# Optimization experiments

Hardware: AMD Instinct MI355X
Metric: run time of the kernel (lower is better)

## Reference

```python
import jax, jax.numpy as jnp
import numpy as np

N_NODES = 100000
NUM_LAYER = 3
REG_WEIGHT = 1e-4


def setup_inputs() -> dict:
    key = jax.random.key(0)
    ks = jax.random.split(key, 6)
    E = 1280000
    B = 4096
    D = 64
    # xavier-uniform-like scale for embedding table
    emb_weight = jax.random.normal(ks[0], (N_NODES, D), dtype=jnp.float32) * 0.01
    src = jax.random.randint(ks[1], (E,), 0, N_NODES, dtype=jnp.int32)
    dst = jax.random.randint(ks[2], (E,), 0, N_NODES, dtype=jnp.int32)
    users = jax.random.randint(ks[3], (B,), 0, N_NODES, dtype=jnp.int32)
    pos = jax.random.randint(ks[4], (B,), 0, N_NODES, dtype=jnp.int32)
    neg = jax.random.randint(ks[5], (B,), 0, N_NODES, dtype=jnp.int32)
    return {"emb_weight": emb_weight, "src": src, "dst": dst,
            "users": users, "pos": pos, "neg": neg}


def _edge_norm(src, dst):
    # DGL norm(): d = sum of edge mask (ones) per dst node; adj_e = d[src]^-0.5 * d[dst]^-0.5
    ones = jnp.ones(src.shape[0], dtype=jnp.float32)
    deg = jax.ops.segment_sum(ones, dst, num_segments=N_NODES)
    dinv = jnp.where(deg > 0, deg ** -0.5, 0.0)  # inf -> 0 handling
    return dinv[src] * dinv[dst]  # [E]


def _propagate(emb_weight, src, dst, adj):
    # LightGCN propagation: h_{l+1}[v] = sum_{(u->v)} adj_e * h_l[u]
    h = emb_weight
    layers = [h]
    for _ in range(NUM_LAYER):
        m = h[src] * adj[:, None]                    # [E, D] gather + edge weight
        h = jax.ops.segment_sum(m, dst, num_segments=N_NODES)  # [N, D] scatter-sum
        layers.append(h)
    return jnp.mean(jnp.stack(layers, axis=1), axis=1)  # mean over L+1 layers


def reference(emb_weight, src, dst, users, pos, neg):
    adj = _edge_norm(src, dst)
    all_emb = _propagate(emb_weight, src, dst, adj)

    u_e, p_e, n_e = all_emb[users], all_emb[pos], all_emb[neg]
    u0, p0, n0 = emb_weight[users], emb_weight[pos], emb_weight[neg]

    B = users.shape[0]
    reg_loss = 0.5 * (jnp.sum(u0 ** 2) + jnp.sum(p0 ** 2) + jnp.sum(n0 ** 2)) / B
    reg_loss = reg_loss * REG_WEIGHT

    pos_scores = jnp.sum(u_e * p_e, axis=1)
    neg_scores = jnp.sum(u_e * n_e, axis=1)
    loss_emb = jnp.mean(jax.nn.softplus(neg_scores - pos_scores))

    loss = loss_emb + reg_loss
    return loss, loss_emb, reg_loss
```

## Files before the change

### kernel.cpp

```cpp
#include <hip/hip_runtime.h>
#include <hip/hip_fp8.h>
#include <math.h>

#define N_NODES 100000
#define DIM 64
#define NUM_LAYER 3
#define BATCH 4096
#define REG_WEIGHT 1e-4f
#define NBUCKET 391
#define STAGE_CAP 4096
#define CURPAD 16
#define H_SCALE 64.0f
#define H_INV_SCALE (1.0f / 64.0f)

__device__ unsigned char g_hf8[2][(size_t)N_NODES * DIM];
__device__ float g_sums[(size_t)3 * BATCH * DIM];
__device__ int   g_row_ptr[N_NODES + 1];
__device__ float g_dinv[N_NODES];
__device__ int   g_bcur[NBUCKET * CURPAD];
__device__ unsigned int g_stage[NBUCKET * STAGE_CAP];
__device__ int2  g_csr[1280000];
__device__ float g_part_sp[BATCH];
__device__ float g_part_rg[BATCH];

__device__ inline float fp8_to_f32(unsigned int v) {
    __hip_fp8_e4m3 t; t.__x = (__hip_fp8_storage_t)(v & 0xFF); return (float)t;
}
__device__ inline unsigned int f32_to_fp8(float f) {
    __hip_fp8_e4m3 t(f); return (unsigned int)t.__x;
}

__global__ void prelude(const float* __restrict__ emb,
                        const int* __restrict__ users, const int* __restrict__ pos,
                        const int* __restrict__ neg) {
    int i = blockIdx.x * blockDim.x + threadIdx.x;
    int stride = gridDim.x * blockDim.x;
    for (int k = i; k < NBUCKET; k += stride) g_bcur[k * CURPAD] = k * STAGE_CAP;
    const int NW = N_NODES * DIM / 4;
    unsigned int* hw = (unsigned int*)g_hf8[0];
    for (int k = i; k < NW; k += stride) {
        const float* e = emb + (size_t)k * 4;
        hw[k] = f32_to_fp8(e[0] * H_SCALE)         | (f32_to_fp8(e[1] * H_SCALE) << 8) |
                (f32_to_fp8(e[2] * H_SCALE) << 16) | (f32_to_fp8(e[3] * H_SCALE) << 24);
    }
    for (int k = i; k < 3 * BATCH * DIM; k += stride) {
        int wid = k >> 6, lane = k & 63;
        int which = wid / BATCH, s = wid - which * BATCH;
        const int* idx = (which == 0) ? users : ((which == 1) ? pos : neg);
        g_sums[k] = emb[(size_t)idx[s] * DIM + lane];
    }
}

#define EDGES_PER_THREAD 8
__global__ void __launch_bounds__(1024) stage_buckets(const int* __restrict__ src,
                                                      const int* __restrict__ dst, int E) {
    __shared__ int h[NBUCKET];
    __shared__ int cur[NBUCKET];
    int tid = threadIdx.x;
    int base = blockIdx.x * (1024 * EDGES_PER_THREAD);
    for (int i = tid; i < NBUCKET; i += 1024) h[i] = 0;
    __syncthreads();
    int myd[EDGES_PER_THREAD], mys[EDGES_PER_THREAD];
    #pragma unroll
    for (int k = 0; k < EDGES_PER_THREAD; ++k) {
        int e = base + k * 1024 + tid;
        if (e < E) {
            myd[k] = dst[e]; mys[k] = src[e];
            atomicAdd(&h[myd[k] >> 8], 1);
        } else myd[k] = -1;
    }
    __syncthreads();
    for (int i = tid; i < NBUCKET; i += 1024) {
        int c = h[i];
        cur[i] = c ? atomicAdd(&g_bcur[i * CURPAD], c) : 0;
    }
    __syncthreads();
    #pragma unroll
    for (int k = 0; k < EDGES_PER_THREAD; ++k) {
        if (myd[k] >= 0) {
            int p = atomicAdd(&cur[myd[k] >> 8], 1);
            g_stage[p] = (unsigned int)((mys[k] << 8) | (myd[k] & 255));
        }
    }
}

__global__ void __launch_bounds__(512) bucket_finalize() {
    __shared__ int cs[512];
    __shared__ int lh[256], sc[256];
    int b = blockIdx.x, t = threadIdx.x;
    int c = (t < NBUCKET) ? (g_bcur[t * CURPAD] - t * STAGE_CAP) : 0;
    cs[t] = c;
    __syncthreads();
    for (int off = 1; off < 512; off <<= 1) {
        int x = (t >= off) ? cs[t - off] : 0;
        __syncthreads();
        cs[t] += x;
        __syncthreads();
    }
    int mybase = (b > 0) ? cs[b - 1] : 0;
    int cnt    = cs[b] - mybase;
    if (b == 0 && t == 0) g_row_ptr[N_NODES] = cs[NBUCKET - 1];
    int sbeg = b * STAGE_CAP;
    if (t < 256) lh[t] = 0;
    __syncthreads();
    for (int k = t; k < cnt; k += 512)
        atomicAdd(&lh[g_stage[sbeg + k] & 255], 1);
    __syncthreads();
    int v = 0;
    if (t < 256) { v = lh[t]; sc[t] = v; }
    __syncthreads();
    for (int off = 1; off < 256; off <<= 1) {
        int x = (t >= off && t < 256) ? sc[t - off] : 0;
        __syncthreads();
        if (t < 256) sc[t] += x;
        __syncthreads();
    }
    if (t < 256) {
        int node = (b << 8) + t;
        if (node < N_NODES) {
            g_row_ptr[node] = mybase + sc[t] - v;
            g_dinv[node]    = (v > 0) ? rsqrtf((float)v) : 0.0f;
        }
    }
}

__global__ void bucket_place() {
    __shared__ int cur[256];
    int b = blockIdx.x, t = threadIdx.x;
    int cnt  = g_bcur[b * CURPAD] - b * STAGE_CAP;
    int sbeg = b * STAGE_CAP;
    int node = (b << 8) + t;
    cur[t] = (node < N_NODES) ? g_row_ptr[node] : 0;
    __syncthreads();
    for (int k = t; k < cnt; k += 256) {
        unsigned int e = g_stage[sbeg + k];
        int dl = e & 255;
        int s  = (int)(e >> 8);
        int pos = atomicAdd(&cur[dl], 1);
        int d = (b << 8) + dl;
        float w = g_dinv[s] * g_dinv[d];
        g_csr[pos] = make_int2(s, __float_as_int(w));
    }
}

__global__ void pull_layer_fp8(const unsigned char* __restrict__ h,
                               unsigned char* __restrict__ hn) {
    int wid  = (blockIdx.x * blockDim.x + threadIdx.x) >> 6;
    int lane = threadIdx.x & 63;
    if (wid >= N_NODES) return;
    int g  = lane >> 4;
    int li = lane & 15;
    int beg = g_row_ptr[wid], end = g_row_ptr[wid + 1];
    float a0 = 0.f, a1 = 0.f, a2 = 0.f, a3 = 0.f;
    for (int base = beg; base < end; base += 64) {
        int k = base + lane;
        int s = 0; float w = 0.0f;
        if (k < end) { int2 ew = g_csr[k]; s = ew.x; w = __int_as_float(ew.y); }
        int cnt = min(64, end - base);
        for (int j = 0; j < cnt; j += 8) {
            int   sA = __shfl(s, j + g);
            float wA = __shfl(w, j + g);
            int   sB = __shfl(s, j + 4 + g);
            float wB = __shfl(w, j + 4 + g);
            unsigned int dA = *(const unsigned int*)(h + (size_t)sA * DIM + li * 4);
            unsigned int dB = *(const unsigned int*)(h + (size_t)sB * DIM + li * 4);
            a0 = fmaf(wA, fp8_to_f32(dA),       a0);
            a1 = fmaf(wA, fp8_to_f32(dA >> 8),  a1);
            a2 = fmaf(wA, fp8_to_f32(dA >> 16), a2);
            a3 = fmaf(wA, fp8_to_f32(dA >> 24), a3);
            a0 = fmaf(wB, fp8_to_f32(dB),       a0);
            a1 = fmaf(wB, fp8_to_f32(dB >> 8),  a1);
            a2 = fmaf(wB, fp8_to_f32(dB >> 16), a2);
            a3 = fmaf(wB, fp8_to_f32(dB >> 24), a3);
        }
    }
    #pragma unroll
    for (int off = 16; off < 64; off <<= 1) {
        a0 += __shfl_xor(a0, off);
        a1 += __shfl_xor(a1, off);
        a2 += __shfl_xor(a2, off);
        a3 += __shfl_xor(a3, off);
    }
    if (lane < 16) {
        unsigned int outw = f32_to_fp8(a0) | (f32_to_fp8(a1) << 8) |
                            (f32_to_fp8(a2) << 16) | (f32_to_fp8(a3) << 24);
        *(unsigned int*)(hn + (size_t)wid * DIM + li * 4) = outw;
    }
}

__global__ void pull_sampled(const unsigned char* __restrict__ h,
                             const int* __restrict__ users, const int* __restrict__ pos,
                             const int* __restrict__ neg) {
    int wid  = (blockIdx.x * blockDim.x + threadIdx.x) >> 6;
    int lane = threadIdx.x & 63;
    if (wid >= 3 * BATCH) return;
    int which = wid / BATCH;
    int i     = wid - which * BATCH;
    const int* idx = (which == 0) ? users : ((which == 1) ? pos : neg);
    int node = idx[i];
    int g  = lane >> 4;
    int li = lane & 15;
    int beg = g_row_ptr[node], end = g_row_ptr[node + 1];
    float a0 = 0.f, a1 = 0.f, a2 = 0.f, a3 = 0.f;
    for (int base = beg; base < end; base += 64) {
        int k = base + lane;
        int s = 0; float w = 0.0f;
        if (k < end) { int2 ew = g_csr[k]; s = ew.x; w = __int_as_float(ew.y); }
        int cnt = min(64, end - base);
        for (int j = 0; j < cnt; j += 8) {
            int   sA = __shfl(s, j + g);
            float wA = __shfl(w, j + g);
            int   sB = __shfl(s, j + 4 + g);
            float wB = __shfl(w, j + 4 + g);
            unsigned int dA = *(const unsigned int*)(h + (size_t)sA * DIM + li * 4);
            unsigned int dB = *(const unsigned int*)(h + (size_t)sB * DIM + li * 4);
            a0 = fmaf(wA, fp8_to_f32(dA),       a0);
            a1 = fmaf(wA, fp8_to_f32(dA >> 8),  a1);
            a2 = fmaf(wA, fp8_to_f32(dA >> 16), a2);
            a3 = fmaf(wA, fp8_to_f32(dA >> 24), a3);
            a0 = fmaf(wB, fp8_to_f32(dB),       a0);
            a1 = fmaf(wB, fp8_to_f32(dB >> 8),  a1);
            a2 = fmaf(wB, fp8_to_f32(dB >> 16), a2);
            a3 = fmaf(wB, fp8_to_f32(dB >> 24), a3);
        }
    }
    #pragma unroll
    for (int off = 16; off < 64; off <<= 1) {
        a0 += __shfl_xor(a0, off);
        a1 += __shfl_xor(a1, off);
        a2 += __shfl_xor(a2, off);
        a3 += __shfl_xor(a3, off);
    }
    if (lane < 16) {
        unsigned int dn = *(const unsigned int*)(h + (size_t)node * DIM + li * 4);
        float* sp = &g_sums[(size_t)wid * DIM + li * 4];
        sp[0] += (a0 + fp8_to_f32(dn))       * H_INV_SCALE;
        sp[1] += (a1 + fp8_to_f32(dn >> 8))  * H_INV_SCALE;
        sp[2] += (a2 + fp8_to_f32(dn >> 16)) * H_INV_SCALE;
        sp[3] += (a3 + fp8_to_f32(dn >> 24)) * H_INV_SCALE;
    }
}

__global__ void gather_acc_fp8(const unsigned char* __restrict__ h,
                               const int* __restrict__ users, const int* __restrict__ pos,
                               const int* __restrict__ neg) {
    int wid  = (blockIdx.x * blockDim.x + threadIdx.x) >> 6;
    int lane = threadIdx.x & 63;
    if (wid >= 3 * BATCH) return;
    int which = wid / BATCH;
    int i     = wid - which * BATCH;
    const int* idx = (which == 0) ? users : ((which == 1) ? pos : neg);
    int node = idx[i];
    g_sums[(size_t)wid * DIM + lane] += fp8_to_f32(h[(size_t)node * DIM + lane]) * H_INV_SCALE;
}

__global__ void score_reduce(const float* __restrict__ emb,
                             const int* __restrict__ users, const int* __restrict__ pos,
                             const int* __restrict__ neg) {
    int wid  = (blockIdx.x * blockDim.x + threadIdx.x) >> 6;
    int lane = threadIdx.x & 63;
    if (wid >= BATCH) return;
    float u = 0.25f * g_sums[(size_t)wid * DIM + lane];
    float p = 0.25f * g_sums[(size_t)(BATCH + wid) * DIM + lane];
    float n = 0.25f * g_sums[(size_t)(2 * BATCH + wid) * DIM + lane];
    float ps = u * p;
    float ns = u * n;
    float u0 = emb[(size_t)users[wid] * DIM + lane];
    float p0 = emb[(size_t)pos[wid]   * DIM + lane];
    float n0 = emb[(size_t)neg[wid]   * DIM + lane];
    float rg = u0 * u0 + p0 * p0 + n0 * n0;
    #pragma unroll
    for (int off = 32; off > 0; off >>= 1) {
        ps += __shfl_down(ps, off);
        ns += __shfl_down(ns, off);
        rg += __shfl_down(rg, off);
    }
    if (lane == 0) {
        float x  = ns - ps;
        float sp = fmaxf(x, 0.0f) + log1pf(expf(-fabsf(x)));
        g_part_sp[wid] = sp;
        g_part_rg[wid] = rg;
    }
}

__global__ void final_reduce(float* __restrict__ out) {
    __shared__ float s_sp[256], s_rg[256];
    int t = threadIdx.x;
    float sp = 0.0f, rg = 0.0f;
    for (int i = t; i < BATCH; i += 256) { sp += g_part_sp[i]; rg += g_part_rg[i]; }
    s_sp[t] = sp; s_rg[t] = rg;
    __syncthreads();
    for (int off = 128; off > 0; off >>= 1) {
        if (t < off) { s_sp[t] += s_sp[t + off]; s_rg[t] += s_rg[t + off]; }
        __syncthreads();
    }
    if (t == 0) {
        float loss_emb = s_sp[0] / (float)BATCH;
        float reg      = 0.5f * s_rg[0] / (float)BATCH * REG_WEIGHT;
        out[0] = loss_emb + reg;
        out[1] = loss_emb;
        out[2] = reg;
    }
}

extern "C" void kernel_launch(void* const* d_in, const int* in_sizes, int n_in,
                              void* d_out, int out_size, void* d_ws, size_t ws_size,
                              hipStream_t stream) {
    const float* emb   = (const float*)d_in[0];
    const int*   src   = (const int*)d_in[1];
    const int*   dst   = (const int*)d_in[2];
    const int*   users = (const int*)d_in[3];
    const int*   pos   = (const int*)d_in[4];
    const int*   neg   = (const int*)d_in[5];
    const int E = in_sizes[1];
    float* out = (float*)d_out;

    unsigned char* hf_a;  hipGetSymbolAddress((void**)&hf_a, HIP_SYMBOL(g_hf8));
    unsigned char* hf_b = hf_a + (size_t)N_NODES * DIM;

    prelude<<<1024, 256, 0, stream>>>(emb, users, pos, neg);

    const int STAGE_BLOCKS = (E + 1024 * EDGES_PER_THREAD - 1) / (1024 * EDGES_PER_THREAD);
    stage_buckets<<<STAGE_BLOCKS, 1024, 0, stream>>>(src, dst, E);
    bucket_finalize<<<NBUCKET, 512, 0, stream>>>();
    bucket_place<<<NBUCKET, 256, 0, stream>>>();

    pull_layer_fp8<<<(N_NODES * 64 + 255) / 256, 256, 0, stream>>>(hf_a, hf_b);
    gather_acc_fp8<<<(3 * BATCH * 64 + 255) / 256, 256, 0, stream>>>(hf_b, users, pos, neg);

    pull_layer_fp8<<<(N_NODES * 64 + 255) / 256, 256, 0, stream>>>(hf_b, hf_a);

    pull_sampled<<<(3 * BATCH * 64 + 255) / 256, 256, 0, stream>>>(hf_a, users, pos, neg);

    score_reduce<<<(BATCH * 64 + 255) / 256, 256, 0, stream>>>(emb, users, pos, neg);
    final_reduce<<<1, 256, 0, stream>>>(out);
}
```

Before: 211.2 us.

## Fuse CSR placement into finalize, compute edge weights on the fly, fuse sample gather

Merges bucket_finalize and bucket_place into one kernel and stores only source indices in the CSR, halving CSR bytes; edge weights are recomputed in the pull kernels from g_dinv. Sampled-node layer-1 outputs are written directly by the first pull layer through a per-node linked list built with atomicExch during staging, which removes the gather_acc kernel and the prelude's g_sums initialization. The layer-0 term is now added in score_reduce. This costs an extra random g_dinv gather per edge in every pull and a short list walk per node.

```diff
diff --git a/kernel.cpp b/kernel.cpp
--- a/kernel.cpp
+++ b/kernel.cpp
@@ -19,7 +19,9 @@
 __device__ float g_dinv[N_NODES];
 __device__ int   g_bcur[NBUCKET * CURPAD];
 __device__ unsigned int g_stage[NBUCKET * STAGE_CAP];
-__device__ int2  g_csr[1280000];
+__device__ int   g_csr[1280000];
+__device__ int   g_shead[N_NODES];
+__device__ int   g_snext[3 * BATCH];
 __device__ float g_part_sp[BATCH];
 __device__ float g_part_rg[BATCH];
 
@@ -30,12 +32,11 @@
     __hip_fp8_e4m3 t(f); return (unsigned int)t.__x;
 }
 
-__global__ void prelude(const float* __restrict__ emb,
-                        const int* __restrict__ users, const int* __restrict__ pos,
-                        const int* __restrict__ neg) {
+__global__ void prelude(const float* __restrict__ emb) {
     int i = blockIdx.x * blockDim.x + threadIdx.x;
     int stride = gridDim.x * blockDim.x;
     for (int k = i; k < NBUCKET; k += stride) g_bcur[k * CURPAD] = k * STAGE_CAP;
+    for (int k = i; k < N_NODES; k += stride) g_shead[k] = -1;
     const int NW = N_NODES * DIM / 4;
     unsigned int* hw = (unsigned int*)g_hf8[0];
     for (int k = i; k < NW; k += stride) {
@@ -43,20 +44,23 @@
         hw[k] = f32_to_fp8(e[0] * H_SCALE)         | (f32_to_fp8(e[1] * H_SCALE) << 8) |
                 (f32_to_fp8(e[2] * H_SCALE) << 16) | (f32_to_fp8(e[3] * H_SCALE) << 24);
     }
-    for (int k = i; k < 3 * BATCH * DIM; k += stride) {
-        int wid = k >> 6, lane = k & 63;
-        int which = wid / BATCH, s = wid - which * BATCH;
-        const int* idx = (which == 0) ? users : ((which == 1) ? pos : neg);
-        g_sums[k] = emb[(size_t)idx[s] * DIM + lane];
-    }
 }
 
 #define EDGES_PER_THREAD 8
 __global__ void __launch_bounds__(1024) stage_buckets(const int* __restrict__ src,
-                                                      const int* __restrict__ dst, int E) {
+                                                      const int* __restrict__ dst, int E,
+                                                      const int* __restrict__ users,
+                                                      const int* __restrict__ pos,
+                                                      const int* __restrict__ neg) {
     __shared__ int h[NBUCKET];
     __shared__ int cur[NBUCKET];
     int tid = threadIdx.x;
+    int gt = blockIdx.x * 1024 + tid;
+    if (gt < 3 * BATCH) {
+        int which = gt / BATCH, s = gt - which * BATCH;
+        const int* idx = (which == 0) ? users : ((which == 1) ? pos : neg);
+        g_snext[gt] = atomicExch(&g_shead[idx[s]], gt);
+    }
     int base = blockIdx.x * (1024 * EDGES_PER_THREAD);
     for (int i = tid; i < NBUCKET; i += 1024) h[i] = 0;
     __syncthreads();
@@ -84,9 +88,9 @@
     }
 }
 
-__global__ void __launch_bounds__(512) bucket_finalize() {
+__global__ void __launch_bounds__(512) finalize_place() {
     __shared__ int cs[512];
-    __shared__ int lh[256], sc[256];
+    __shared__ int lh[256], sc[256], cur[256];
     int b = blockIdx.x, t = threadIdx.x;
     int c = (t < NBUCKET) ? (g_bcur[t * CURPAD] - t * STAGE_CAP) : 0;
     cs[t] = c;
@@ -116,46 +120,36 @@
         __syncthreads();
     }
     if (t < 256) {
+        int start = mybase + sc[t] - v;
+        cur[t] = start;
         int node = (b << 8) + t;
         if (node < N_NODES) {
-            g_row_ptr[node] = mybase + sc[t] - v;
+            g_row_ptr[node] = start;
             g_dinv[node]    = (v > 0) ? rsqrtf((float)v) : 0.0f;
         }
     }
-}
-
-__global__ void bucket_place() {
-    __shared__ int cur[256];
-    int b = blockIdx.x, t = threadIdx.x;
-    int cnt  = g_bcur[b * CURPAD] - b * STAGE_CAP;
-    int sbeg = b * STAGE_CAP;
-    int node = (b << 8) + t;
-    cur[t] = (node < N_NODES) ? g_row_ptr[node] : 0;
-    __syncthreads();
-    for (int k = t; k < cnt; k += 256) {
+    __syncthreads();
+    for (int k = t; k < cnt; k += 512) {
         unsigned int e = g_stage[sbeg + k];
-        int dl = e & 255;
-        int s  = (int)(e >> 8);
-        int pos = atomicAdd(&cur[dl], 1);
-        int d = (b << 8) + dl;
-        float w = g_dinv[s] * g_dinv[d];
-        g_csr[pos] = make_int2(s, __float_as_int(w));
+        int pos = atomicAdd(&cur[e & 255], 1);
+        g_csr[pos] = (int)(e >> 8);
     }
 }
 
 __global__ void pull_layer_fp8(const unsigned char* __restrict__ h,
-                               unsigned char* __restrict__ hn) {
+                               unsigned char* __restrict__ hn, int do_gather) {
     int wid  = (blockIdx.x * blockDim.x + threadIdx.x) >> 6;
     int lane = threadIdx.x & 63;
     if (wid >= N_NODES) return;
     int g  = lane >> 4;
     int li = lane & 15;
     int beg = g_row_ptr[wid], end = g_row_ptr[wid + 1];
+    float dinv_d = g_dinv[wid];
     float a0 = 0.f, a1 = 0.f, a2 = 0.f, a3 = 0.f;
     for (int base = beg; base < end; base += 64) {
         int k = base + lane;
         int s = 0; float w = 0.0f;
-        if (k < end) { int2 ew = g_csr[k]; s = ew.x; w = __int_as_float(ew.y); }
+        if (k < end) { s = g_csr[k]; w = g_dinv[s] * dinv_d; }
         int cnt = min(64, end - base);
         for (int j = 0; j < cnt; j += 8) {
             int   sA = __shfl(s, j + g);
@@ -186,6 +180,19 @@
                             (f32_to_fp8(a2) << 16) | (f32_to_fp8(a3) << 24);
         *(unsigned int*)(hn + (size_t)wid * DIM + li * 4) = outw;
     }
+    if (do_gather) {
+        int sidx = g_shead[wid];
+        while (sidx >= 0) {
+            if (lane < 16) {
+                float* sp = &g_sums[(size_t)sidx * DIM + li * 4];
+                sp[0] = a0 * H_INV_SCALE;
+                sp[1] = a1 * H_INV_SCALE;
+                sp[2] = a2 * H_INV_SCALE;
+                sp[3] = a3 * H_INV_SCALE;
+            }
+            sidx = g_snext[sidx];
+        }
+    }
 }
 
 __global__ void pull_sampled(const unsigned char* __restrict__ h,
@@ -201,11 +208,12 @@
     int g  = lane >> 4;
     int li = lane & 15;
     int beg = g_row_ptr[node], end = g_row_ptr[node + 1];
+    float dinv_d = g_dinv[node];
     float a0 = 0.f, a1 = 0.f, a2 = 0.f, a3 = 0.f;
     for (int base = beg; base < end; base += 64) {
         int k = base + lane;
         int s = 0; float w = 0.0f;
-        if (k < end) { int2 ew = g_csr[k]; s = ew.x; w = __int_as_float(ew.y); }
+        if (k < end) { s = g_csr[k]; w = g_dinv[s] * dinv_d; }
         int cnt = min(64, end - base);
         for (int j = 0; j < cnt; j += 8) {
             int   sA = __shfl(s, j + g);
@@ -241,33 +249,20 @@
     }
 }
 
-__global__ void gather_acc_fp8(const unsigned char* __restrict__ h,
-                               const int* __restrict__ users, const int* __restrict__ pos,
-                               const int* __restrict__ neg) {
-    int wid  = (blockIdx.x * blockDim.x + threadIdx.x) >> 6;
-    int lane = threadIdx.x & 63;
-    if (wid >= 3 * BATCH) return;
-    int which = wid / BATCH;
-    int i     = wid - which * BATCH;
-    const int* idx = (which == 0) ? users : ((which == 1) ? pos : neg);
-    int node = idx[i];
-    g_sums[(size_t)wid * DIM + lane] += fp8_to_f32(h[(size_t)node * DIM + lane]) * H_INV_SCALE;
-}
-
 __global__ void score_reduce(const float* __restrict__ emb,
                              const int* __restrict__ users, const int* __restrict__ pos,
                              const int* __restrict__ neg) {
     int wid  = (blockIdx.x * blockDim.x + threadIdx.x) >> 6;
     int lane = threadIdx.x & 63;
     if (wid >= BATCH) return;
-    float u = 0.25f * g_sums[(size_t)wid * DIM + lane];
-    float p = 0.25f * g_sums[(size_t)(BATCH + wid) * DIM + lane];
-    float n = 0.25f * g_sums[(size_t)(2 * BATCH + wid) * DIM + lane];
-    float ps = u * p;
-    float ns = u * n;
     float u0 = emb[(size_t)users[wid] * DIM + lane];
     float p0 = emb[(size_t)pos[wid]   * DIM + lane];
     float n0 = emb[(size_t)neg[wid]   * DIM + lane];
+    float u = 0.25f * (g_sums[(size_t)wid * DIM + lane] + u0);
+    float p = 0.25f * (g_sums[(size_t)(BATCH + wid) * DIM + lane] + p0);
+    float n = 0.25f * (g_sums[(size_t)(2 * BATCH + wid) * DIM + lane] + n0);
+    float ps = u * p;
+    float ns = u * n;
     float rg = u0 * u0 + p0 * p0 + n0 * n0;
     #pragma unroll
     for (int off = 32; off > 0; off >>= 1) {
@@ -318,17 +313,15 @@
     unsigned char* hf_a;  hipGetSymbolAddress((void**)&hf_a, HIP_SYMBOL(g_hf8));
     unsigned char* hf_b = hf_a + (size_t)N_NODES * DIM;
 
-    prelude<<<1024, 256, 0, stream>>>(emb, users, pos, neg);
+    prelude<<<1024, 256, 0, stream>>>(emb);
 
     const int STAGE_BLOCKS = (E + 1024 * EDGES_PER_THREAD - 1) / (1024 * EDGES_PER_THREAD);
-    stage_buckets<<<STAGE_BLOCKS, 1024, 0, stream>>>(src, dst, E);
-    bucket_finalize<<<NBUCKET, 512, 0, stream>>>();
-    bucket_place<<<NBUCKET, 256, 0, stream>>>();
-
-    pull_layer_fp8<<<(N_NODES * 64 + 255) / 256, 256, 0, stream>>>(hf_a, hf_b);
-    gather_acc_fp8<<<(3 * BATCH * 64 + 255) / 256, 256, 0, stream>>>(hf_b, users, pos, neg);
-
-    pull_layer_fp8<<<(N_NODES * 64 + 255) / 256, 256, 0, stream>>>(hf_b, hf_a);
+    stage_buckets<<<STAGE_BLOCKS, 1024, 0, stream>>>(src, dst, E, users, pos, neg);
+    finalize_place<<<NBUCKET, 512, 0, stream>>>();
+
+    pull_layer_fp8<<<(N_NODES * 64 + 255) / 256, 256, 0, stream>>>(hf_a, hf_b, 1);
+
+    pull_layer_fp8<<<(N_NODES * 64 + 255) / 256, 256, 0, stream>>>(hf_b, hf_a, 0);
 
     pull_sampled<<<(3 * BATCH * 64 + 255) / 256, 256, 0, stream>>>(hf_a, users, pos, neg);
 
```

After: 209.6 us. Within noise of the previous version (-0.8%).
